# Performance work log

Measured on AMD Instinct MI355X. Metric: run time of the kernel, lower is better.

Reference implementation:

```python
import jax, jax.numpy as jnp
import numpy as np

B, D_IN, D_Z, D_H, D_T, D_REC = 8192, 1024, 256, 256, 16, 256


def _softplus_beta(x, beta):
    # torch F.softplus(x, beta) = (1/beta) * log(1 + exp(beta*x))
    return jax.nn.softplus(beta * x) / beta


def setup_inputs() -> dict:
    key = jax.random.key(0)
    ks = jax.random.split(key, 17)
    w = lambda k, o, i: jax.random.normal(k, (o, i), jnp.float32) * (1.0 / np.sqrt(i))
    return {
        "I_t": jax.random.uniform(ks[0], (B, D_IN), jnp.float32),
        "h_m_1": jax.random.uniform(ks[1], (B, D_H), jnp.float32),
        "z_m_1": jax.random.uniform(ks[2], (B, D_Z), jnp.float32),
        "theta_m_1": jax.random.normal(ks[3], (B, D_T), jnp.float32),
        "eps_z": jax.random.normal(ks[4], (B, D_Z), jnp.float32),
        "eps_zhat": jax.random.normal(ks[5], (B, D_Z), jnp.float32),
        "W_post_mu": w(ks[6], D_Z, D_IN),
        "W_post_lv": w(ks[7], D_Z, D_IN),
        "W_z2h": w(ks[8], D_H, D_Z),
        "W_h2h": w(ks[9], D_H, D_H),
        "W_prior_mu": w(ks[10], D_Z, D_H),
        "W_prior_lv": w(ks[11], D_Z, D_H),
        "W_i2t": w(ks[12], D_T, D_IN),
        "W_vip2t": w(ks[13], D_T, D_Z),
        "W_t2z": w(ks[14], D_Z, D_T),
        "W_rec1": w(ks[15], D_REC, D_Z),
        "W_rec2": w(ks[16], D_IN, D_REC),
    }


def reference(I_t, h_m_1, z_m_1, theta_m_1, eps_z, eps_zhat,
              W_post_mu, W_post_lv, W_z2h, W_h2h, W_prior_mu, W_prior_lv,
              W_i2t, W_vip2t, W_t2z, W_rec1, W_rec2):
    relu = jax.nn.relu
    # prior pathway (perception_only=True branch)
    mu_p = relu(h_m_1 @ W_prior_mu.T)                       # [B, D_Z]
    sigma_p = _softplus_beta(h_m_1 @ W_prior_lv.T, 1.2)     # [B, D_Z]
    # theta dynamics; vip_to_theta has Positive parametrization -> relu(W)
    theta_h = (0.5 * theta_m_1 + 0.1 * (I_t @ W_i2t.T)
               - jax.lax.stop_gradient(sigma_p) @ relu(W_vip2t).T)  # [B, D_T]
    theta = 0.001 * _softplus_beta(theta_h, 0.5)
    # posterior + reparameterized sample
    mu_q = relu(I_t @ W_post_mu.T)
    sigma_q = relu(I_t @ W_post_lv.T)
    raw_z = jnp.clip(mu_q + eps_z * sigma_q, 0.0, 1.0)
    thresholds = 10.0 * (theta @ relu(W_t2z).T)             # Positive parametrization
    z = relu(raw_z - thresholds)                            # [B, D_Z]
    # reconstruction (two bias-free linears + sigmoid)
    I_hat = jax.nn.sigmoid((z @ W_rec1.T) @ W_rec2.T)       # [B, D_IN]
    # higher-state update and prior sample
    h = relu(z_m_1 @ W_z2h.T + h_m_1 @ W_h2h.T)             # [B, D_H]
    z_hat = mu_p + eps_zhat * sigma_p                       # [B, D_Z]
    # losses (as in torch forward)
    spatial = jnp.mean((I_t - I_hat) ** 2)
    temporal = jnp.mean((jax.lax.stop_gradient(z) - z_hat) ** 2)
    energy = jnp.mean(jnp.abs(z))
    return (I_hat, z, h, z_hat, spatial, temporal, energy)
```

## Files before the change

kernel.cpp:

```cpp
#include <hip/hip_runtime.h>
#include <math.h>

#define BB 8192
#define DIN 1024
#define DZ 256
#define DH 256
#define DT 16
#define DREC 256

#define OFF_IHAT 0
#define OFF_Z    (BB * DIN)
#define OFF_H    (OFF_Z + BB * DZ)
#define OFF_ZHAT (OFF_H + BB * DH)
#define OFF_SCAL (OFF_ZHAT + BB * DZ)

#define WS_HBF   0
#define WS_ZM1   2097152
#define WS_W     4194304
#define W_PM  (WS_W + 0)
#define W_PL  (W_PM + 262144)
#define W_Z2H (W_PL + 262144)
#define W_H2H (W_Z2H + 65536)
#define W_PRM (W_H2H + 65536)
#define W_PRL (W_PRM + 65536)
#define W_I2T (W_PRL + 65536)
#define W_VIP (W_I2T + 16384)
#define W_R1  (W_VIP + 4096)
#define W_R2  (W_R1 + 65536)
#define WS_ENDW  (W_R2 + 262144)
#define WS_SIGMA WS_ENDW
#define WS_ZBF   (WS_SIGMA + 2097152)
#define WS_R1BF  (WS_ZBF + 2097152)

typedef unsigned short u16;
typedef __attribute__((ext_vector_type(8))) unsigned short u16x8;
typedef __attribute__((ext_vector_type(8))) __bf16 bf16x8;
typedef __attribute__((ext_vector_type(4))) float f32x4;

#define MFMA __builtin_amdgcn_mfma_f32_16x16x32_bf16

__device__ inline u16 f2bf(float f) {
  unsigned u = __builtin_bit_cast(unsigned, f);
  u += 0x7fff + ((u >> 16) & 1);
  return (u16)(u >> 16);
}
__device__ inline float softplus_stable(float y) {
  return (y > 20.f) ? y : log1pf(expf(y));
}
__device__ inline bf16x8 gf(const u16* p) {
  return __builtin_bit_cast(bf16x8, *(const u16x8*)p);
}
__device__ inline f32x4 fzero() { return (f32x4){0.f, 0.f, 0.f, 0.f}; }

__device__ inline float block_sum256(float v, float* rbuf) {
#pragma unroll
  for (int off = 32; off > 0; off >>= 1) v += __shfl_down(v, off, 64);
  __syncthreads();
  if ((threadIdx.x & 63) == 0) rbuf[threadIdx.x >> 6] = v;
  __syncthreads();
  return rbuf[0] + rbuf[1] + rbuf[2] + rbuf[3];
}
__device__ inline float block_sum512(float v, float* rbuf) {
#pragma unroll
  for (int off = 32; off > 0; off >>= 1) v += __shfl_down(v, off, 64);
  __syncthreads();
  if ((threadIdx.x & 63) == 0) rbuf[threadIdx.x >> 6] = v;
  __syncthreads();
  float s = 0.f;
#pragma unroll
  for (int i = 0; i < 8; ++i) s += rbuf[i];
  return s;
}

__device__ inline void decode4(int id, int rows, int& row0, int& col0) {
  int xcd = id & 7, t = id >> 3;
  col0 = (t & 3) * 64;
  row0 = ((t >> 2) * 8 + xcd) * rows;
}

__device__ inline void dmaA32(u16* tile, const u16* __restrict__ gsrc,
                              int row0, int ldk, int k0) {
  const int lane = threadIdx.x & 63, w = threadIdx.x >> 6;
  int rb = w * 8;
  int r = rb + (lane >> 3);
  int gl = (lane & 7) ^ (r & 7);
  const u16* src = gsrc + (size_t)(row0 + r) * ldk + k0 + gl * 8;
  u16* dst = tile + rb * 64;
  __builtin_amdgcn_global_load_lds(
      (const __attribute__((address_space(1))) unsigned int*)(const void*)src,
      (__attribute__((address_space(3))) unsigned int*)(void*)dst, 16, 0, 0);
}
__device__ inline void dmaB64(u16* tile, const u16* __restrict__ gsrc,
                              int row0, int ldk, int k0) {
  const int lane = threadIdx.x & 63, w = threadIdx.x >> 6;
#pragma unroll
  for (int c = 0; c < 2; ++c) {
    int rb = w * 16 + c * 8;
    int r = rb + (lane >> 3);
    int gl = (lane & 7) ^ (r & 7);
    const u16* src = gsrc + (size_t)(row0 + r) * ldk + k0 + gl * 8;
    u16* dst = tile + rb * 64;
    __builtin_amdgcn_global_load_lds(
        (const __attribute__((address_space(1))) unsigned int*)(const void*)src,
        (__attribute__((address_space(3))) unsigned int*)(void*)dst, 16, 0, 0);
  }
}
__device__ inline bf16x8 rd(const u16* tile, int r, int gl) {
  return gf(tile + r * 64 + ((gl ^ (r & 7)) * 8));
}

__device__ inline void stg64x128(u16* tile, const u16* __restrict__ g,
                                 int row0, int ldk, int k0) {
  const int lane = threadIdx.x & 63, w = threadIdx.x >> 6;
#pragma unroll
  for (int i = 0; i < 2; ++i) {
    int rb = (w * 2 + i) * 4;
    int r = rb + (lane >> 4);
    int d = lane & 15;
    int s = d ^ (r & 7);
    const u16* src = g + (size_t)(row0 + r) * ldk + k0 + s * 8;
    u16* dst = tile + rb * 128;
    __builtin_amdgcn_global_load_lds(
        (const __attribute__((address_space(1))) unsigned int*)(const void*)src,
        (__attribute__((address_space(3))) unsigned int*)(void*)dst, 16, 0, 0);
  }
}
__device__ inline void stg16x128(u16* tile, const u16* __restrict__ g,
                                 int ldk, int k0) {
  const int lane = threadIdx.x & 63, w = threadIdx.x >> 6;
  if (w < 4) {
    int rb = w * 4;
    int r = rb + (lane >> 4);
    int d = lane & 15;
    int s = d ^ (r & 7);
    const u16* src = g + (size_t)r * ldk + k0 + s * 8;
    u16* dst = tile + rb * 128;
    __builtin_amdgcn_global_load_lds(
        (const __attribute__((address_space(1))) unsigned int*)(const void*)src,
        (__attribute__((address_space(3))) unsigned int*)(void*)dst, 16, 0, 0);
  }
}
__device__ inline bf16x8 rd128(const u16* tile, int r, int j) {
  return gf(tile + r * 128 + ((j ^ (r & 7)) * 8));
}

__device__ inline void lda4(bf16x8 (&ar)[4], const u16* base, int kwin,
                            int fq) {
#pragma unroll
  for (int kk = 0; kk < 4; ++kk) ar[kk] = gf(base + kwin + kk * 32 + fq * 8);
}
__device__ inline void cmpMain(const u16* buf, bf16x8 (&ar)[4], f32x4 (&mu)[4],
                               f32x4 (&sg)[4], f32x4& tt, int frow, int fq) {
#pragma unroll
  for (int kk = 0; kk < 4; ++kk) {
    int j = kk * 4 + fq;
#pragma unroll
    for (int n = 0; n < 4; ++n) {
      mu[n] = MFMA(ar[kk], rd128(buf, n * 16 + frow, j), mu[n], 0, 0, 0);
      sg[n] = MFMA(ar[kk], rd128(buf + 8192, n * 16 + frow, j), sg[n], 0, 0, 0);
    }
    tt = MFMA(ar[kk], rd128(buf + 16384, frow, j), tt, 0, 0, 0);
  }
}
__device__ inline void cmpSig(const u16* buf, bf16x8 (&ar)[4], f32x4& tt,
                              int frow, int fq) {
#pragma unroll
  for (int kk = 0; kk < 4; ++kk)
    tt = MFMA(ar[kk], rd128(buf + 16384, frow, kk * 4 + fq), tt, 0, 0, 0);
}
__device__ inline void hpCmp3(const u16* buf, bf16x8 (&ar)[4], f32x4 (&ah)[4],
                              f32x4 (&am)[4], f32x4 (&as_)[4], int frow,
                              int fq) {
#pragma unroll
  for (int kk = 0; kk < 4; ++kk) {
    int j = kk * 4 + fq;
#pragma unroll
    for (int n = 0; n < 4; ++n) {
      ah[n]  = MFMA(ar[kk], rd128(buf, n * 16 + frow, j), ah[n], 0, 0, 0);
      am[n]  = MFMA(ar[kk], rd128(buf + 8192, n * 16 + frow, j), am[n], 0, 0, 0);
      as_[n] = MFMA(ar[kk], rd128(buf + 16384, n * 16 + frow, j), as_[n], 0, 0, 0);
    }
  }
}
__device__ inline void hpCmp1(const u16* buf, bf16x8 (&ar)[4], f32x4 (&ah)[4],
                              int frow, int fq) {
#pragma unroll
  for (int kk = 0; kk < 4; ++kk) {
    int j = kk * 4 + fq;
#pragma unroll
    for (int n = 0; n < 4; ++n)
      ah[n] = MFMA(ar[kk], rd128(buf, n * 16 + frow, j), ah[n], 0, 0, 0);
  }
}

__global__ __launch_bounds__(256) void k_cvt(
    const float* __restrict__ I_t, const float* __restrict__ h_m_1,
    const float* __restrict__ z_m_1, const float* __restrict__ Wpm,
    const float* __restrict__ Wpl, const float* __restrict__ Wz2h,
    const float* __restrict__ Wh2h, const float* __restrict__ Wprm,
    const float* __restrict__ Wprl, const float* __restrict__ Wi2t,
    const float* __restrict__ Wv, const float* __restrict__ Wr1,
    const float* __restrict__ Wr2, u16* __restrict__ dstI,
    u16* __restrict__ dstW) {
  const int S1 = 8388608, S2 = 10485760, S3 = 12582912, S4 = 12845056,
            S5 = 13107200, S6 = 13172736, S7 = 13238272, S8 = 13303808,
            S9 = 13369344, S10 = 13385728, S11 = 13389824, S12 = 13455360,
            S13 = 13717504;
  int nchunk = S13 / 8;
  for (int c = blockIdx.x * 256 + threadIdx.x; c < nchunk;
       c += gridDim.x * 256) {
    int f = c * 8;
    const float* src;
    float scale = 1.f;
    bool nrelu = false;
    u16* dst;
    if (f < S1) {
      src = I_t + f;
      dst = dstI + f;
    } else {
      dst = dstW + (f - S1);
      if (f < S2)       src = h_m_1 + (f - S1);
      else if (f < S3)  src = z_m_1 + (f - S2);
      else if (f < S4)  src = Wpm + (f - S3);
      else if (f < S5)  src = Wpl + (f - S4);
      else if (f < S6)  src = Wz2h + (f - S5);
      else if (f < S7)  src = Wh2h + (f - S6);
      else if (f < S8)  src = Wprm + (f - S7);
      else if (f < S9)  src = Wprl + (f - S8);
      else if (f < S10) { src = Wi2t + (f - S9);  scale = 0.1f; }
      else if (f < S11) { src = Wv + (f - S10);   nrelu = true; }
      else if (f < S12) src = Wr1 + (f - S11);
      else              src = Wr2 + (f - S12);
    }
    float4 v0 = *(const float4*)(src);
    float4 v1 = *(const float4*)(src + 4);
    float vals[8] = {v0.x, v0.y, v0.z, v0.w, v1.x, v1.y, v1.z, v1.w};
    u16x8 o;
#pragma unroll
    for (int j = 0; j < 8; ++j) {
      float x = vals[j];
      x = nrelu ? -fmaxf(x, 0.f) : x * scale;
      o[j] = f2bf(x);
    }
    *(u16x8*)(dst) = o;
  }
}

__global__ __launch_bounds__(512, 2) void k_hp(
    const u16* __restrict__ h_bf, const u16* __restrict__ zm1,
    const u16* __restrict__ Wh2h, const u16* __restrict__ Wprm,
    const u16* __restrict__ Wprl, const u16* __restrict__ Wz2h,
    const float* __restrict__ eps_zhat, float* __restrict__ h_out,
    float* __restrict__ zhat_out, u16* __restrict__ sigma_bf) {
  __shared__ __align__(16) u16 smem[2 * 24576];
  const int tid = threadIdx.x, lane = tid & 63, w = tid >> 6;
  const int frow = lane & 15, fq = lane >> 4;
  int row0, col0;
  {
    int xcd = blockIdx.x & 7, t = blockIdx.x >> 3;
    col0 = (t & 3) * 64;
    row0 = ((t >> 2) * 8 + xcd) * 128;
  }
  u16* b0 = smem;
  u16* b1 = smem + 24576;

  f32x4 ah[4], am[4], as_[4];
#pragma unroll
  for (int n = 0; n < 4; ++n) { ah[n] = fzero(); am[n] = fzero(); as_[n] = fzero(); }

  const u16* Ah = h_bf + (size_t)(row0 + w * 16 + frow) * DH;
  const u16* Az = zm1 + (size_t)(row0 + w * 16 + frow) * DZ;
  bf16x8 arA[4], arB[4];

  stg64x128(b0, Wh2h, col0, DH, 0);
  stg64x128(b0 + 8192, Wprm, col0, DH, 0);
  stg64x128(b0 + 16384, Wprl, col0, DH, 0);
  lda4(arA, Ah, 0, fq);
  __syncthreads();
  stg64x128(b1, Wh2h, col0, DH, 128);
  stg64x128(b1 + 8192, Wprm, col0, DH, 128);
  stg64x128(b1 + 16384, Wprl, col0, DH, 128);
  lda4(arB, Ah, 128, fq);
  hpCmp3(b0, arA, ah, am, as_, frow, fq);
  __syncthreads();
  stg64x128(b0, Wz2h, col0, DZ, 0);
  lda4(arA, Az, 0, fq);
  hpCmp3(b1, arB, ah, am, as_, frow, fq);
  __syncthreads();
  stg64x128(b1, Wz2h, col0, DZ, 128);
  lda4(arB, Az, 128, fq);
  hpCmp1(b0, arA, ah, frow, fq);
  __syncthreads();
  hpCmp1(b1, arB, ah, frow, fq);

  float* ht = (float*)smem;
  float* mt = (float*)(smem + 8448);
  float* st = (float*)(smem + 16896);
#pragma unroll 1
  for (int p = 0; p < 2; ++p) {
    __syncthreads();
    if ((w >> 2) == p) {
#pragma unroll
      for (int n = 0; n < 4; ++n)
#pragma unroll
        for (int r = 0; r < 4; ++r) {
          int lrl = (w & 3) * 16 + fq * 4 + r;
          int ln = n * 16 + frow;
          ht[lrl * 66 + ln] = fmaxf(ah[n][r], 0.f);
          mt[lrl * 66 + ln] = fmaxf(am[n][r], 0.f);
          st[lrl * 66 + ln] = softplus_stable(1.2f * as_[n][r]) * (1.f / 1.2f);
        }
    }
    __syncthreads();
    int lr2 = tid >> 3, c0 = (tid & 7) * 8;
    int m2 = row0 + p * 64 + lr2;
    float h8[8], mu8[8], sg8[8];
#pragma unroll
    for (int j = 0; j < 8; ++j) {
      h8[j] = ht[lr2 * 66 + c0 + j];
      mu8[j] = mt[lr2 * 66 + c0 + j];
      sg8[j] = st[lr2 * 66 + c0 + j];
    }
    float* hp = h_out + (size_t)m2 * DH + col0 + c0;
    *(float4*)hp = make_float4(h8[0], h8[1], h8[2], h8[3]);
    *(float4*)(hp + 4) = make_float4(h8[4], h8[5], h8[6], h8[7]);
    const float* ep = eps_zhat + (size_t)m2 * DZ + col0 + c0;
    float4 e0 = ((const float4*)ep)[0], e1 = ((const float4*)ep)[1];
    float e8[8] = {e0.x, e0.y, e0.z, e0.w, e1.x, e1.y, e1.z, e1.w};
    float zh8[8];
    u16x8 sb;
#pragma unroll
    for (int j = 0; j < 8; ++j) {
      zh8[j] = mu8[j] + e8[j] * sg8[j];
      sb[j] = f2bf(sg8[j]);
    }
    float* zp = zhat_out + (size_t)m2 * DZ + col0 + c0;
    *(float4*)zp = make_float4(zh8[0], zh8[1], zh8[2], zh8[3]);
    *(float4*)(zp + 4) = make_float4(zh8[4], zh8[5], zh8[6], zh8[7]);
    *(u16x8*)(sigma_bf + (size_t)m2 * DZ + col0 + c0) = sb;
  }
}

__global__ __launch_bounds__(512, 2) void k_post(
    const u16* __restrict__ I_bf, const u16* __restrict__ Wpm,
    const u16* __restrict__ Wpl, const u16* __restrict__ Wi2t,
    const u16* __restrict__ Wv, const u16* __restrict__ sigma_bf,
    const float* __restrict__ theta_m_1, const float* __restrict__ W_t2z,
    const float* __restrict__ eps_z, const float* __restrict__ zhat,
    float* __restrict__ z_out, u16* __restrict__ z_bf,
    float* __restrict__ scal) {
  __shared__ __align__(16) u16 smem[2 * 18432];
  __shared__ float thwt[128 * 17 + 64 * 17];
  __shared__ float rbuf[8];
  const int tid = threadIdx.x, lane = tid & 63, w = tid >> 6;
  const int frow = lane & 15, fq = lane >> 4;
  int row0, col0;
  {
    int xcd = blockIdx.x & 7, t = blockIdx.x >> 3;
    col0 = (t & 3) * 64;
    row0 = ((t >> 2) * 8 + xcd) * 128;
  }
  u16* b0 = smem;
  u16* b1 = smem + 18432;

  f32x4 mu[4], sg[4], tt = fzero();
#pragma unroll
  for (int i = 0; i < 4; ++i) { mu[i] = fzero(); sg[i] = fzero(); }

  const u16* Abase = I_bf + (size_t)(row0 + w * 16 + frow) * DIN;
  const u16* Sbase = sigma_bf + (size_t)(row0 + w * 16 + frow) * DZ;
  bf16x8 arA[4], arB[4];

#define STGM(buf, k0)                           \
  stg64x128(buf, Wpm, col0, DIN, k0);           \
  stg64x128((buf) + 8192, Wpl, col0, DIN, k0);  \
  stg16x128((buf) + 16384, Wi2t, DIN, k0)

  STGM(b0, 0);
  lda4(arA, Abase, 0, fq);
  __syncthreads(); STGM(b1, 128); lda4(arB, Abase, 128, fq);
  cmpMain(b0, arA, mu, sg, tt, frow, fq);
  __syncthreads(); STGM(b0, 256); lda4(arA, Abase, 256, fq);
  cmpMain(b1, arB, mu, sg, tt, frow, fq);
  __syncthreads(); STGM(b1, 384); lda4(arB, Abase, 384, fq);
  cmpMain(b0, arA, mu, sg, tt, frow, fq);
  __syncthreads(); STGM(b0, 512); lda4(arA, Abase, 512, fq);
  cmpMain(b1, arB, mu, sg, tt, frow, fq);
  __syncthreads(); STGM(b1, 640); lda4(arB, Abase, 640, fq);
  cmpMain(b0, arA, mu, sg, tt, frow, fq);
  __syncthreads(); STGM(b0, 768); lda4(arA, Abase, 768, fq);
  cmpMain(b1, arB, mu, sg, tt, frow, fq);
  __syncthreads(); STGM(b1, 896); lda4(arB, Abase, 896, fq);
  cmpMain(b0, arA, mu, sg, tt, frow, fq);
  __syncthreads(); stg16x128(b0 + 16384, Wv, DZ, 0); lda4(arA, Sbase, 0, fq);
  cmpMain(b1, arB, mu, sg, tt, frow, fq);
  __syncthreads(); stg16x128(b1 + 16384, Wv, DZ, 128); lda4(arB, Sbase, 128, fq);
  cmpSig(b0, arA, tt, frow, fq);
  __syncthreads();
  cmpSig(b1, arB, tt, frow, fq);
#undef STGM

  __syncthreads();
  float* mt   = (float*)smem;
  float* st   = (float*)(smem + 16896);
  float* th_s = thwt;
  float* wt_s = thwt + 128 * 17;

#pragma unroll
  for (int r = 0; r < 4; ++r) {
    int lr = w * 16 + fq * 4 + r;
    float th = 0.5f * theta_m_1[(size_t)(row0 + lr) * DT + frow] + tt[r];
    th_s[lr * 17 + frow] = 0.002f * softplus_stable(0.5f * th);
  }
  for (int idx = tid; idx < 64 * 16; idx += 512) {
    int n = idx >> 4, j = idx & 15;
    wt_s[n * 17 + j] = 10.f * fmaxf(W_t2z[(col0 + n) * DT + j], 0.f);
  }
#pragma unroll
  for (int n = 0; n < 4; ++n)
#pragma unroll
    for (int r = 0; r < 4; ++r) {
      int lr = w * 16 + fq * 4 + r;
      int ln = n * 16 + frow;
      mt[lr * 66 + ln] = fmaxf(mu[n][r], 0.f);
      st[lr * 66 + ln] = fmaxf(sg[n][r], 0.f);
    }
  __syncthreads();
  float tsum = 0.f, esum = 0.f;
  {
    int lr2 = tid >> 2, c0 = (tid & 3) * 16;
    int m2 = row0 + lr2;
    float thv[16];
#pragma unroll
    for (int j = 0; j < 16; ++j) thv[j] = th_s[lr2 * 17 + j];
#pragma unroll
    for (int gb = 0; gb < 2; ++gb) {
      int c = c0 + gb * 8;
      float mu8[8], sg8[8];
#pragma unroll
      for (int j = 0; j < 8; ++j) {
        mu8[j] = mt[lr2 * 66 + c + j];
        sg8[j] = st[lr2 * 66 + c + j];
      }
      const float* ep = eps_z + (size_t)m2 * DZ + col0 + c;
      float4 e0 = ((const float4*)ep)[0], e1 = ((const float4*)ep)[1];
      float e8[8] = {e0.x, e0.y, e0.z, e0.w, e1.x, e1.y, e1.z, e1.w};
      float z8[8];
#pragma unroll
      for (int j = 0; j < 8; ++j) {
        float raw = mu8[j] + e8[j] * sg8[j];
        raw = fminf(fmaxf(raw, 0.f), 1.f);
        float thr = 0.f;
#pragma unroll
        for (int jj = 0; jj < 16; ++jj)
          thr = fmaf(thv[jj], wt_s[(c + j) * 17 + jj], thr);
        z8[j] = fmaxf(raw - thr, 0.f);
      }
      float* zp = z_out + (size_t)m2 * DZ + col0 + c;
      *(float4*)zp = make_float4(z8[0], z8[1], z8[2], z8[3]);
      *(float4*)(zp + 4) = make_float4(z8[4], z8[5], z8[6], z8[7]);
      u16x8 zb;
#pragma unroll
      for (int j = 0; j < 8; ++j) zb[j] = f2bf(z8[j]);
      *(u16x8*)(z_bf + (size_t)m2 * DZ + col0 + c) = zb;
      const float* zhp = zhat + (size_t)m2 * DZ + col0 + c;
      float4 h0 = ((const float4*)zhp)[0], h1 = ((const float4*)zhp)[1];
      float zh8[8] = {h0.x, h0.y, h0.z, h0.w, h1.x, h1.y, h1.z, h1.w};
#pragma unroll
      for (int j = 0; j < 8; ++j) {
        float d = z8[j] - zh8[j];
        tsum += d * d;
        esum += z8[j];
      }
    }
  }
  float t = block_sum512(tsum, rbuf);
  if (tid == 0) atomicAdd(scal + 1, t * (1.f / ((float)BB * DZ)));
  float e = block_sum512(esum, rbuf);
  if (tid == 0) atomicAdd(scal + 2, e * (1.f / ((float)BB * DZ)));
}

__global__ __launch_bounds__(256, 4) void k_rec1(const u16* __restrict__ z_bf,
                                                 const u16* __restrict__ Wr1,
                                                 u16* __restrict__ r1_bf) {
  __shared__ __align__(16) u16 smem[2048 + 4096];
  u16* As = smem;
  u16* B0s = smem + 2048;
  const int tid = threadIdx.x, lane = tid & 63, w = tid >> 6;
  const int frow = lane & 15, fq = lane >> 4;
  const int wr = w & 1, wc = w >> 1;
  int row0, col0;
  decode4(blockIdx.x, 32, row0, col0);
  f32x4 acc[2] = {fzero(), fzero()};
  for (int k0 = 0; k0 < DZ; k0 += 64) {
    __syncthreads();
    dmaA32(As, z_bf, row0, DZ, k0);
    dmaB64(B0s, Wr1, col0, DZ, k0);
    __syncthreads();
#pragma unroll
    for (int ks = 0; ks < 2; ++ks) {
      bf16x8 a = rd(As, wr * 16 + frow, ks * 4 + fq);
#pragma unroll
      for (int ni = 0; ni < 2; ++ni)
        acc[ni] = MFMA(a, rd(B0s, wc * 32 + ni * 16 + frow, ks * 4 + fq),
                       acc[ni], 0, 0, 0);
    }
  }
  __syncthreads();
  float* rt = (float*)smem;
#pragma unroll
  for (int ni = 0; ni < 2; ++ni)
#pragma unroll
    for (int r = 0; r < 4; ++r) {
      int lr = wr * 16 + fq * 4 + r;
      int ln = wc * 32 + ni * 16 + frow;
      rt[lr * 66 + ln] = acc[ni][r];
    }
  __syncthreads();
  {
    int lr2 = tid >> 3, c0 = (tid & 7) * 8;
    int m2 = row0 + lr2;
    u16x8 rb;
#pragma unroll
    for (int j = 0; j < 8; ++j) rb[j] = f2bf(rt[lr2 * 66 + c0 + j]);
    *(u16x8*)(r1_bf + (size_t)m2 * DREC + col0 + c0) = rb;
  }
}

__global__ __launch_bounds__(256, 4) void k_rec2(const u16* __restrict__ r1_bf,
                                                 const u16* __restrict__ Wr2,
                                                 const float* __restrict__ I_t,
                                                 float* __restrict__ ihat_out,
                                                 float* __restrict__ scal) {
  __shared__ __align__(16) u16 smem[4096 + 4096];
  u16* As = smem;
  u16* B0s = smem + 4096;
  __shared__ float rbuf[4];
  const int tid = threadIdx.x, lane = tid & 63, w = tid >> 6;
  const int frow = lane & 15, fq = lane >> 4;
  int row0, col0;
  {
    int id = blockIdx.x;
    int xcd = id & 7, t = id >> 3;
    col0 = (t & 15) * 64;
    row0 = ((t >> 4) * 8 + xcd) * 64;
  }
  f32x4 acc[4] = {fzero(), fzero(), fzero(), fzero()};
  for (int k0 = 0; k0 < DREC; k0 += 64) {
    __syncthreads();
    dmaB64(As, r1_bf, row0, DREC, k0);
    dmaB64(B0s, Wr2, col0, DREC, k0);
    __syncthreads();
#pragma unroll
    for (int ks = 0; ks < 2; ++ks) {
      bf16x8 a = rd(As, w * 16 + frow, ks * 4 + fq);
#pragma unroll
      for (int ni = 0; ni < 4; ++ni)
        acc[ni] = MFMA(a, rd(B0s, ni * 16 + frow, ks * 4 + fq), acc[ni], 0, 0, 0);
    }
  }
  float lsum = 0.f;
  float* it = (float*)smem;
#pragma unroll 1
  for (int p = 0; p < 2; ++p) {
    __syncthreads();
    if ((w >> 1) == p) {
#pragma unroll
      for (int ni = 0; ni < 4; ++ni)
#pragma unroll
        for (int r = 0; r < 4; ++r) {
          int lrl = (w & 1) * 16 + fq * 4 + r;
          int ln = ni * 16 + frow;
          it[lrl * 66 + ln] = 1.f / (1.f + expf(-acc[ni][r]));
        }
    }
    __syncthreads();
    int lr2 = tid >> 3, c0 = (tid & 7) * 8;
    int m2 = row0 + p * 32 + lr2;
    float i8[8];
#pragma unroll
    for (int j = 0; j < 8; ++j) i8[j] = it[lr2 * 66 + c0 + j];
    float* op = ihat_out + (size_t)m2 * DIN + col0 + c0;
    *(float4*)op = make_float4(i8[0], i8[1], i8[2], i8[3]);
    *(float4*)(op + 4) = make_float4(i8[4], i8[5], i8[6], i8[7]);
    const float* ip = I_t + (size_t)m2 * DIN + col0 + c0;
    float4 a0 = ((const float4*)ip)[0], a1 = ((const float4*)ip)[1];
    float t8[8] = {a0.x, a0.y, a0.z, a0.w, a1.x, a1.y, a1.z, a1.w};
#pragma unroll
    for (int j = 0; j < 8; ++j) {
      float d = t8[j] - i8[j];
      lsum += d * d;
    }
  }
  float s = block_sum256(lsum, rbuf);
  if (tid == 0) atomicAdd(scal + 0, s * (1.f / ((float)BB * DIN)));
}

extern "C" void kernel_launch(void* const* d_in, const int* in_sizes, int n_in,
                              void* d_out, int out_size, void* d_ws,
                              size_t ws_size, hipStream_t stream) {
  const float* I_t       = (const float*)d_in[0];
  const float* h_m_1     = (const float*)d_in[1];
  const float* z_m_1     = (const float*)d_in[2];
  const float* theta_m_1 = (const float*)d_in[3];
  const float* eps_z     = (const float*)d_in[4];
  const float* eps_zhat  = (const float*)d_in[5];
  const float* W_post_mu = (const float*)d_in[6];
  const float* W_post_lv = (const float*)d_in[7];
  const float* W_z2h     = (const float*)d_in[8];
  const float* W_h2h     = (const float*)d_in[9];
  const float* W_prior_mu= (const float*)d_in[10];
  const float* W_prior_lv= (const float*)d_in[11];
  const float* W_i2t     = (const float*)d_in[12];
  const float* W_vip2t   = (const float*)d_in[13];
  const float* W_t2z     = (const float*)d_in[14];
  const float* W_rec1    = (const float*)d_in[15];
  const float* W_rec2    = (const float*)d_in[16];

  float* out = (float*)d_out;
  float* ihat = out + OFF_IHAT;
  float* zout = out + OFF_Z;
  float* hout = out + OFF_H;
  float* zhat = out + OFF_ZHAT;
  float* scal = out + OFF_SCAL;

  u16* ws_u = (u16*)d_ws;
  u16* I_bf = (u16*)ihat;
  u16* h_bf = ws_u + WS_HBF;
  u16* zm1_bf = ws_u + WS_ZM1;
  u16* sigma_bf = ws_u + WS_SIGMA;
  u16* z_bf = ws_u + WS_ZBF;
  u16* r1_bf = ws_u + WS_R1BF;

  hipMemsetAsync(scal, 0, 3 * sizeof(float), stream);

  k_cvt<<<2048, 256, 0, stream>>>(I_t, h_m_1, z_m_1, W_post_mu, W_post_lv,
                                  W_z2h, W_h2h, W_prior_mu, W_prior_lv, W_i2t,
                                  W_vip2t, W_rec1, W_rec2, I_bf, ws_u + WS_HBF);

  k_hp<<<256, 512, 0, stream>>>(h_bf, zm1_bf, ws_u + W_H2H, ws_u + W_PRM,
                                ws_u + W_PRL, ws_u + W_Z2H, eps_zhat, hout,
                                zhat, sigma_bf);
  k_post<<<256, 512, 0, stream>>>(I_bf, ws_u + W_PM, ws_u + W_PL,
                                  ws_u + W_I2T, ws_u + W_VIP, sigma_bf,
                                  theta_m_1, W_t2z, eps_z, zhat, zout, z_bf,
                                  scal);
  k_rec1<<<1024, 256, 0, stream>>>(z_bf, ws_u + W_R1, r1_bf);
  k_rec2<<<2048, 256, 0, stream>>>(r1_bf, ws_u + W_R2, I_t, ihat, scal);
}
```

Measured before the change: 236.9 us.

## Retile reconstruction GEMMs to 128-row blocks with register-held A and double-buffered B

Both reconstruction GEMM kernels move to 512-thread blocks covering 128 rows, reusing the stg64x128/lda4/hpCmp1 helpers from the earlier kernels. The A operand is loaded straight into registers and the weight tile is staged through two LDS buffers over 128-wide K chunks, replacing the old 64-wide K loop with a sync before and after every step. The aim is fewer barriers, more reuse of each weight tile, and fewer block launches. In exchange, each block uses more registers and LDS, so occupancy drops and there are fewer blocks to hide latency.

```diff
diff --git a/kernel.cpp b/kernel.cpp
--- a/kernel.cpp
+++ b/kernel.cpp
@@ -70,43 +70,6 @@
 #pragma unroll
   for (int i = 0; i < 8; ++i) s += rbuf[i];
   return s;
-}
-
-__device__ inline void decode4(int id, int rows, int& row0, int& col0) {
-  int xcd = id & 7, t = id >> 3;
-  col0 = (t & 3) * 64;
-  row0 = ((t >> 2) * 8 + xcd) * rows;
-}
-
-__device__ inline void dmaA32(u16* tile, const u16* __restrict__ gsrc,
-                              int row0, int ldk, int k0) {
-  const int lane = threadIdx.x & 63, w = threadIdx.x >> 6;
-  int rb = w * 8;
-  int r = rb + (lane >> 3);
-  int gl = (lane & 7) ^ (r & 7);
-  const u16* src = gsrc + (size_t)(row0 + r) * ldk + k0 + gl * 8;
-  u16* dst = tile + rb * 64;
-  __builtin_amdgcn_global_load_lds(
-      (const __attribute__((address_space(1))) unsigned int*)(const void*)src,
-      (__attribute__((address_space(3))) unsigned int*)(void*)dst, 16, 0, 0);
-}
-__device__ inline void dmaB64(u16* tile, const u16* __restrict__ gsrc,
-                              int row0, int ldk, int k0) {
-  const int lane = threadIdx.x & 63, w = threadIdx.x >> 6;
-#pragma unroll
-  for (int c = 0; c < 2; ++c) {
-    int rb = w * 16 + c * 8;
-    int r = rb + (lane >> 3);
-    int gl = (lane & 7) ^ (r & 7);
-    const u16* src = gsrc + (size_t)(row0 + r) * ldk + k0 + gl * 8;
-    u16* dst = tile + rb * 64;
-    __builtin_amdgcn_global_load_lds(
-        (const __attribute__((address_space(1))) unsigned int*)(const void*)src,
-        (__attribute__((address_space(3))) unsigned int*)(void*)dst, 16, 0, 0);
-  }
-}
-__device__ inline bf16x8 rd(const u16* tile, int r, int gl) {
-  return gf(tile + r * 64 + ((gl ^ (r & 7)) * 8));
 }
 
 __device__ inline void stg64x128(u16* tile, const u16* __restrict__ g,
@@ -480,119 +443,131 @@
   if (tid == 0) atomicAdd(scal + 2, e * (1.f / ((float)BB * DZ)));
 }
 
-__global__ __launch_bounds__(256, 4) void k_rec1(const u16* __restrict__ z_bf,
+__global__ __launch_bounds__(512, 2) void k_rec1(const u16* __restrict__ z_bf,
                                                  const u16* __restrict__ Wr1,
                                                  u16* __restrict__ r1_bf) {
-  __shared__ __align__(16) u16 smem[2048 + 4096];
-  u16* As = smem;
-  u16* B0s = smem + 2048;
+  __shared__ __align__(16) u16 smem[2 * 9216];
   const int tid = threadIdx.x, lane = tid & 63, w = tid >> 6;
   const int frow = lane & 15, fq = lane >> 4;
-  const int wr = w & 1, wc = w >> 1;
   int row0, col0;
-  decode4(blockIdx.x, 32, row0, col0);
-  f32x4 acc[2] = {fzero(), fzero()};
-  for (int k0 = 0; k0 < DZ; k0 += 64) {
-    __syncthreads();
-    dmaA32(As, z_bf, row0, DZ, k0);
-    dmaB64(B0s, Wr1, col0, DZ, k0);
-    __syncthreads();
-#pragma unroll
-    for (int ks = 0; ks < 2; ++ks) {
-      bf16x8 a = rd(As, wr * 16 + frow, ks * 4 + fq);
-#pragma unroll
-      for (int ni = 0; ni < 2; ++ni)
-        acc[ni] = MFMA(a, rd(B0s, wc * 32 + ni * 16 + frow, ks * 4 + fq),
-                       acc[ni], 0, 0, 0);
-    }
-  }
-  __syncthreads();
+  {
+    int xcd = blockIdx.x & 7, t = blockIdx.x >> 3;
+    col0 = (t & 3) * 64;
+    row0 = ((t >> 2) * 8 + xcd) * 128;
+  }
+  u16* b0 = smem;
+  u16* b1 = smem + 9216;
+
+  f32x4 acc[4];
+#pragma unroll
+  for (int n = 0; n < 4; ++n) acc[n] = fzero();
+
+  const u16* Abase = z_bf + (size_t)(row0 + w * 16 + frow) * DZ;
+  bf16x8 arA[4], arB[4];
+
+  stg64x128(b0, Wr1, col0, DZ, 0);
+  lda4(arA, Abase, 0, fq);
+  __syncthreads();
+  stg64x128(b1, Wr1, col0, DZ, 128);
+  lda4(arB, Abase, 128, fq);
+  hpCmp1(b0, arA, acc, frow, fq);
+  __syncthreads();
+  hpCmp1(b1, arB, acc, frow, fq);
+  __syncthreads();
+
   float* rt = (float*)smem;
 #pragma unroll
-  for (int ni = 0; ni < 2; ++ni)
+  for (int n = 0; n < 4; ++n)
 #pragma unroll
     for (int r = 0; r < 4; ++r) {
-      int lr = wr * 16 + fq * 4 + r;
-      int ln = wc * 32 + ni * 16 + frow;
-      rt[lr * 66 + ln] = acc[ni][r];
+      int lr = w * 16 + fq * 4 + r;
+      int ln = n * 16 + frow;
+      rt[lr * 66 + ln] = acc[n][r];
     }
   __syncthreads();
   {
-    int lr2 = tid >> 3, c0 = (tid & 7) * 8;
+    int lr2 = tid >> 2, c0 = (tid & 3) * 16;
     int m2 = row0 + lr2;
-    u16x8 rb;
-#pragma unroll
-    for (int j = 0; j < 8; ++j) rb[j] = f2bf(rt[lr2 * 66 + c0 + j]);
-    *(u16x8*)(r1_bf + (size_t)m2 * DREC + col0 + c0) = rb;
-  }
-}
-
-__global__ __launch_bounds__(256, 4) void k_rec2(const u16* __restrict__ r1_bf,
+    u16* dst = r1_bf + (size_t)m2 * DREC + col0 + c0;
+#pragma unroll
+    for (int gb = 0; gb < 2; ++gb) {
+      u16x8 rb;
+#pragma unroll
+      for (int j = 0; j < 8; ++j) rb[j] = f2bf(rt[lr2 * 66 + c0 + gb * 8 + j]);
+      *(u16x8*)(dst + gb * 8) = rb;
+    }
+  }
+}
+
+__global__ __launch_bounds__(512, 2) void k_rec2(const u16* __restrict__ r1_bf,
                                                  const u16* __restrict__ Wr2,
                                                  const float* __restrict__ I_t,
                                                  float* __restrict__ ihat_out,
                                                  float* __restrict__ scal) {
-  __shared__ __align__(16) u16 smem[4096 + 4096];
-  u16* As = smem;
-  u16* B0s = smem + 4096;
-  __shared__ float rbuf[4];
+  __shared__ __align__(16) u16 smem[2 * 9216];
+  __shared__ float rbuf[8];
   const int tid = threadIdx.x, lane = tid & 63, w = tid >> 6;
   const int frow = lane & 15, fq = lane >> 4;
   int row0, col0;
   {
-    int id = blockIdx.x;
-    int xcd = id & 7, t = id >> 3;
+    int xcd = blockIdx.x & 7, t = blockIdx.x >> 3;
     col0 = (t & 15) * 64;
-    row0 = ((t >> 4) * 8 + xcd) * 64;
-  }
-  f32x4 acc[4] = {fzero(), fzero(), fzero(), fzero()};
-  for (int k0 = 0; k0 < DREC; k0 += 64) {
-    __syncthreads();
-    dmaB64(As, r1_bf, row0, DREC, k0);
-    dmaB64(B0s, Wr2, col0, DREC, k0);
-    __syncthreads();
-#pragma unroll
-    for (int ks = 0; ks < 2; ++ks) {
-      bf16x8 a = rd(As, w * 16 + frow, ks * 4 + fq);
-#pragma unroll
-      for (int ni = 0; ni < 4; ++ni)
-        acc[ni] = MFMA(a, rd(B0s, ni * 16 + frow, ks * 4 + fq), acc[ni], 0, 0, 0);
-    }
-  }
+    row0 = ((t >> 4) * 8 + xcd) * 128;
+  }
+  u16* b0 = smem;
+  u16* b1 = smem + 9216;
+
+  f32x4 acc[4];
+#pragma unroll
+  for (int n = 0; n < 4; ++n) acc[n] = fzero();
+
+  const u16* Abase = r1_bf + (size_t)(row0 + w * 16 + frow) * DREC;
+  bf16x8 arA[4], arB[4];
+
+  stg64x128(b0, Wr2, col0, DREC, 0);
+  lda4(arA, Abase, 0, fq);
+  __syncthreads();
+  stg64x128(b1, Wr2, col0, DREC, 128);
+  lda4(arB, Abase, 128, fq);
+  hpCmp1(b0, arA, acc, frow, fq);
+  __syncthreads();
+  hpCmp1(b1, arB, acc, frow, fq);
+  __syncthreads();
+
+  float* it = (float*)smem;
+#pragma unroll
+  for (int n = 0; n < 4; ++n)
+#pragma unroll
+    for (int r = 0; r < 4; ++r) {
+      int lr = w * 16 + fq * 4 + r;
+      int ln = n * 16 + frow;
+      it[lr * 66 + ln] = 1.f / (1.f + expf(-acc[n][r]));
+    }
+  __syncthreads();
   float lsum = 0.f;
-  float* it = (float*)smem;
-#pragma unroll 1
-  for (int p = 0; p < 2; ++p) {
-    __syncthreads();
-    if ((w >> 1) == p) {
-#pragma unroll
-      for (int ni = 0; ni < 4; ++ni)
-#pragma unroll
-        for (int r = 0; r < 4; ++r) {
-          int lrl = (w & 1) * 16 + fq * 4 + r;
-          int ln = ni * 16 + frow;
-          it[lrl * 66 + ln] = 1.f / (1.f + expf(-acc[ni][r]));
-        }
-    }
-    __syncthreads();
-    int lr2 = tid >> 3, c0 = (tid & 7) * 8;
-    int m2 = row0 + p * 32 + lr2;
-    float i8[8];
-#pragma unroll
-    for (int j = 0; j < 8; ++j) i8[j] = it[lr2 * 66 + c0 + j];
+  {
+    int lr2 = tid >> 2, c0 = (tid & 3) * 16;
+    int m2 = row0 + lr2;
     float* op = ihat_out + (size_t)m2 * DIN + col0 + c0;
-    *(float4*)op = make_float4(i8[0], i8[1], i8[2], i8[3]);
-    *(float4*)(op + 4) = make_float4(i8[4], i8[5], i8[6], i8[7]);
     const float* ip = I_t + (size_t)m2 * DIN + col0 + c0;
-    float4 a0 = ((const float4*)ip)[0], a1 = ((const float4*)ip)[1];
-    float t8[8] = {a0.x, a0.y, a0.z, a0.w, a1.x, a1.y, a1.z, a1.w};
-#pragma unroll
-    for (int j = 0; j < 8; ++j) {
-      float d = t8[j] - i8[j];
-      lsum += d * d;
-    }
-  }
-  float s = block_sum256(lsum, rbuf);
+#pragma unroll
+    for (int gb = 0; gb < 2; ++gb) {
+      float i8[8];
+#pragma unroll
+      for (int j = 0; j < 8; ++j) i8[j] = it[lr2 * 66 + c0 + gb * 8 + j];
+      *(float4*)(op + gb * 8) = make_float4(i8[0], i8[1], i8[2], i8[3]);
+      *(float4*)(op + gb * 8 + 4) = make_float4(i8[4], i8[5], i8[6], i8[7]);
+      float4 a0 = ((const float4*)(ip + gb * 8))[0];
+      float4 a1 = ((const float4*)(ip + gb * 8))[1];
+      float t8[8] = {a0.x, a0.y, a0.z, a0.w, a1.x, a1.y, a1.z, a1.w};
+#pragma unroll
+      for (int j = 0; j < 8; ++j) {
+        float d = t8[j] - i8[j];
+        lsum += d * d;
+      }
+    }
+  }
+  float s = block_sum512(lsum, rbuf);
   if (tid == 0) atomicAdd(scal + 0, s * (1.f / ((float)BB * DIN)));
 }
 
@@ -645,6 +620,6 @@
                                   ws_u + W_I2T, ws_u + W_VIP, sigma_bf,
                                   theta_m_1, W_t2z, eps_z, zhat, zout, z_bf,
                                   scal);
-  k_rec1<<<1024, 256, 0, stream>>>(z_bf, ws_u + W_R1, r1_bf);
-  k_rec2<<<2048, 256, 0, stream>>>(r1_bf, ws_u + W_R2, I_t, ihat, scal);
-}
+  k_rec1<<<256, 512, 0, stream>>>(z_bf, ws_u + W_R1, r1_bf);
+  k_rec2<<<1024, 512, 0, stream>>>(r1_bf, ws_u + W_R2, I_t, ihat, scal);
+}
```

Result: faster. 228.3 us (-3.6%).
